# Optimization experiments

Hardware: AMD Instinct MI355X
Metric: run time of the kernel (lower is better)

## Reference

```python
import jax, jax.numpy as jnp
import numpy as np

B, T, D, K = 64, 4096, 128, 512

def setup_inputs() -> dict:
    key = jax.random.key(0)
    k1, k2, k3 = jax.random.split(key, 3)
    embeddings = jax.random.normal(k1, (B, T, D), dtype=jnp.float32)
    mask = jax.random.bernoulli(k2, 0.9, (B, T))
    W = jax.random.normal(k3, (D,), dtype=jnp.float32) * (1.0 / np.sqrt(D))
    b = jnp.zeros((1,), dtype=jnp.float32)
    return {"embeddings": embeddings, "mask": mask, "k": K, "W": W, "b": b}

def reference(embeddings, mask, k, W, b):
    batch, T, dim = embeddings.shape
    if k >= T:
        return embeddings, mask
    # linear score head: (B,T,D) @ (D,) + b -> (B,T)
    scores = jnp.einsum("btd,d->bt", embeddings, W) + b[0]
    neg_inf = jnp.array(-jnp.inf, dtype=scores.dtype)
    scores = jnp.where(mask, scores, neg_inf)
    soft_scores = jax.nn.sigmoid(scores)  # sigmoid(-inf) == 0
    _, topk_idx = jax.lax.top_k(scores, k)          # (B, k)
    topk_idx_sorted = jnp.sort(topk_idx, axis=1)    # preserve original token order
    rows = jnp.arange(batch)[:, None]
    hard_mask = jnp.zeros_like(scores).at[rows, topk_idx].set(1.0)
    # straight-through estimator: hard forward, soft gradient
    ste_mask = hard_mask - jax.lax.stop_gradient(soft_scores) + soft_scores
    weighted = embeddings * ste_mask[:, :, None]
    selected = jnp.take_along_axis(weighted, topk_idx_sorted[:, :, None], axis=1)  # (B,k,D)
    selected_mask = jnp.take_along_axis(mask, topk_idx_sorted, axis=1)             # (B,k)
    return selected, selected_mask
```

## Files before the change

kernel.cpp:

```cpp
#include <hip/hip_runtime.h>
#include <hip/hip_bf16.h>

#define BB 64
#define TT 4096
#define DD 128
#define KK 512

__global__ __launch_bounds__(256) void k_scores(
    const float* __restrict__ emb, const int* __restrict__ mask,
    const float* __restrict__ W, const float* __restrict__ bias,
    float* __restrict__ scores)
{
    const int wave = threadIdx.x >> 6;
    const int lane = threadIdx.x & 63;
    const int half = lane >> 5;
    const int sub  = lane & 31;
    const int pair0 = (blockIdx.x * 4 + wave) * 8;

    const float4 w = ((const float4*)W)[sub];
    const double w0 = (double)w.x, w1 = (double)w.y, w2 = (double)w.z, w3 = (double)w.w;
    const double b0 = (double)bias[0];

#pragma unroll
    for (int i = 0; i < 8; ++i) {
        const int t = (pair0 + i) * 2 + half;
        const float4 e = ((const float4*)emb)[(size_t)t * 32 + sub];
        double s = (double)e.x * w0 + (double)e.y * w1
                 + (double)e.z * w2 + (double)e.w * w3;
        s += __shfl_xor(s, 16, 64);
        s += __shfl_xor(s,  8, 64);
        s += __shfl_xor(s,  4, 64);
        s += __shfl_xor(s,  2, 64);
        s += __shfl_xor(s,  1, 64);
        if (sub == 0) {
            const float val = (float)(s + b0);
            scores[t] = mask[t] ? val : __uint_as_float(0xFF800000u);
        }
    }
}

__device__ __forceinline__ unsigned int block_incl_prefix(
    unsigned int v, int tid, volatile unsigned int* wsum)
{
    const int lane = tid & 63, wv = tid >> 6;
#pragma unroll
    for (int off = 1; off < 64; off <<= 1) {
        const unsigned int u = __shfl_up(v, off, 64);
        if (lane >= off) v += u;
    }
    if (lane == 63) wsum[wv] = v;
    __syncthreads();
    unsigned int add = 0;
    for (int w = 0; w < wv; ++w) add += wsum[w];
    v += add;
    __syncthreads();
    return v;
}

__global__ __launch_bounds__(256) void k_select(
    const float* __restrict__ scores, const int* __restrict__ mask,
    int* __restrict__ idx_out, float* __restrict__ mask_out)
{
    __shared__ unsigned int keys[TT];
    __shared__ unsigned int hist4[4][256];
    __shared__ unsigned int wsum[4];
    __shared__ unsigned int bcast[2];

    const int row = blockIdx.x;
    const int tid = threadIdx.x;
    const int wv  = tid >> 6;
    const float* srow = scores + (size_t)row * TT;
    const int*   mrow = mask   + (size_t)row * TT;

#pragma unroll
    for (int i = 0; i < 16; ++i) {
        const int t = tid * 16 + i;
        const unsigned int u = __float_as_uint(srow[t]);
        keys[t] = (u & 0x80000000u) ? ~u : (u | 0x80000000u);
    }

    unsigned int prefix = 0;
    unsigned int count_above = 0;
    for (int pass = 0; pass < 4; ++pass) {
        const int shift = 24 - 8 * pass;
#pragma unroll
        for (int w = 0; w < 4; ++w) hist4[w][tid] = 0;
        __syncthreads();
#pragma unroll
        for (int i = 0; i < 16; ++i) {
            const unsigned int k = keys[tid * 16 + i];
            const bool in_group = (pass == 0) || ((k >> (shift + 8)) == prefix);
            if (in_group) atomicAdd(&hist4[wv][(k >> shift) & 0xFFu], 1u);
        }
        __syncthreads();
        const unsigned int bin = 255u - (unsigned int)tid;
        const unsigned int h = hist4[0][bin] + hist4[1][bin]
                             + hist4[2][bin] + hist4[3][bin];
        const unsigned int incl = block_incl_prefix(h, tid, wsum);
        const unsigned int excl = incl - h;
        if (count_above + incl >= KK && count_above + excl < KK) {
            bcast[0] = bin;
            bcast[1] = count_above + excl;
        }
        __syncthreads();
        prefix = (prefix << 8) | bcast[0];
        count_above = bcast[1];
        __syncthreads();
    }
    const unsigned int vstar = prefix;
    const unsigned int need  = KK - count_above;

    unsigned int gt = 0, eq = 0;
#pragma unroll
    for (int i = 0; i < 16; ++i) {
        const unsigned int k = keys[tid * 16 + i];
        gt += (k > vstar);
        eq += (k == vstar);
    }
    const unsigned int packed = (gt << 16) | eq;
    const unsigned int incl2 = block_incl_prefix(packed, tid, wsum);
    const unsigned int before = incl2 - packed;
    unsigned int gt_b = before >> 16;
    unsigned int eq_b = before & 0xFFFFu;
#pragma unroll
    for (int i = 0; i < 16; ++i) {
        const int t = tid * 16 + i;
        const unsigned int k = keys[t];
        if (k > vstar) {
            const unsigned int pos = gt_b + (eq_b < need ? eq_b : need);
            idx_out[row * KK + pos]  = t;
            mask_out[row * KK + pos] = mrow[t] ? 1.0f : 0.0f;
            gt_b++;
        } else if (k == vstar) {
            if (eq_b < need) {
                const unsigned int pos = gt_b + eq_b;
                idx_out[row * KK + pos]  = t;
                mask_out[row * KK + pos] = mrow[t] ? 1.0f : 0.0f;
            }
            eq_b++;
        }
    }
}

__global__ __launch_bounds__(256) void k_gather(
    const float* __restrict__ emb, const int* __restrict__ idx,
    float* __restrict__ out)
{
    const int gp   = blockIdx.x * 8 + (threadIdx.x >> 5);
    const int lane = threadIdx.x & 31;
    const int b = gp >> 9;
    const int t = idx[gp];
    const float4* src = (const float4*)(emb + ((size_t)b * TT + t) * DD);
    float4*       dst = (float4*)(out + (size_t)gp * DD);
    dst[lane] = src[lane];
}

extern "C" void kernel_launch(void* const* d_in, const int* in_sizes, int n_in,
                              void* d_out, int out_size, void* d_ws, size_t ws_size,
                              hipStream_t stream)
{
    const float* emb  = (const float*)d_in[0];
    const int*   mask = (const int*)d_in[1];
    const float* W    = (const float*)d_in[3];
    const float* bias = (const float*)d_in[4];

    float* out_sel  = (float*)d_out;
    float* out_mask = (float*)d_out + (size_t)BB * KK * DD;

    float* scores = (float*)d_ws;
    int*   idx    = (int*)((char*)d_ws + (size_t)BB * TT * sizeof(float));

    k_scores<<<BB * TT / 64, 256, 0, stream>>>(emb, mask, W, bias, scores);
    k_select<<<BB, 256, 0, stream>>>(scores, mask, idx, out_mask);
    k_gather<<<BB * KK / 8, 256, 0, stream>>>(emb, idx, out_sel);
}
```

Baseline: 219.7 us.

## Widen radix-select block to 1024 threads and precompute sortable keys in score kernel

The score kernel now writes order-preserving unsigned keys directly, with masked tokens mapped to the key for -inf, so the select kernel no longer converts floats. The select kernel runs with 1024 threads per row, each handling 4 keys loaded as a single uint4. It uses 16 per-wave padded histograms reduced into one, and a single-wave scan over 256 bins. It also drops one barrier per pass. The aim is to cut the serial per-thread work in the 64-block select stage, which badly underfills the GPU, at the cost of more histogram reduction work and contention.

```diff
diff --git a/kernel.cpp b/kernel.cpp
--- a/kernel.cpp
+++ b/kernel.cpp
@@ -6,10 +6,12 @@
 #define DD 128
 #define KK 512
 
+#define KEY_NEG_INF 0x007FFFFFu
+
 __global__ __launch_bounds__(256) void k_scores(
     const float* __restrict__ emb, const int* __restrict__ mask,
     const float* __restrict__ W, const float* __restrict__ bias,
-    float* __restrict__ scores)
+    unsigned int* __restrict__ keys_out)
 {
     const int wave = threadIdx.x >> 6;
     const int lane = threadIdx.x & 63;
@@ -34,97 +36,111 @@
         s += __shfl_xor(s,  1, 64);
         if (sub == 0) {
             const float val = (float)(s + b0);
-            scores[t] = mask[t] ? val : __uint_as_float(0xFF800000u);
+            const unsigned int u = __float_as_uint(val);
+            unsigned int key = (u & 0x80000000u) ? ~u : (u | 0x80000000u);
+            if (!mask[t]) key = KEY_NEG_INF;
+            keys_out[t] = key;
         }
     }
 }
 
-__device__ __forceinline__ unsigned int block_incl_prefix(
-    unsigned int v, int tid, volatile unsigned int* wsum)
-{
-    const int lane = tid & 63, wv = tid >> 6;
-#pragma unroll
-    for (int off = 1; off < 64; off <<= 1) {
-        const unsigned int u = __shfl_up(v, off, 64);
-        if (lane >= off) v += u;
-    }
-    if (lane == 63) wsum[wv] = v;
-    __syncthreads();
-    unsigned int add = 0;
-    for (int w = 0; w < wv; ++w) add += wsum[w];
-    v += add;
-    __syncthreads();
-    return v;
-}
-
-__global__ __launch_bounds__(256) void k_select(
-    const float* __restrict__ scores, const int* __restrict__ mask,
+__global__ __launch_bounds__(1024) void k_select(
+    const unsigned int* __restrict__ keys_in, const int* __restrict__ mask,
     int* __restrict__ idx_out, float* __restrict__ mask_out)
 {
     __shared__ unsigned int keys[TT];
-    __shared__ unsigned int hist4[4][256];
-    __shared__ unsigned int wsum[4];
+    __shared__ unsigned int hist[16][257];
+    __shared__ unsigned int hist_final[256];
+    __shared__ unsigned int wsum[16];
     __shared__ unsigned int bcast[2];
 
-    const int row = blockIdx.x;
-    const int tid = threadIdx.x;
-    const int wv  = tid >> 6;
-    const float* srow = scores + (size_t)row * TT;
-    const int*   mrow = mask   + (size_t)row * TT;
+    const int row  = blockIdx.x;
+    const int tid  = threadIdx.x;
+    const int wv   = tid >> 6;
+    const int lane = tid & 63;
+    const unsigned int* krow = keys_in + (size_t)row * TT;
+    const int*          mrow = mask    + (size_t)row * TT;
 
-#pragma unroll
-    for (int i = 0; i < 16; ++i) {
-        const int t = tid * 16 + i;
-        const unsigned int u = __float_as_uint(srow[t]);
-        keys[t] = (u & 0x80000000u) ? ~u : (u | 0x80000000u);
-    }
+    const uint4 kv = ((const uint4*)krow)[tid];
+    ((uint4*)keys)[tid] = kv;
 
     unsigned int prefix = 0;
     unsigned int count_above = 0;
     for (int pass = 0; pass < 4; ++pass) {
         const int shift = 24 - 8 * pass;
-#pragma unroll
-        for (int w = 0; w < 4; ++w) hist4[w][tid] = 0;
+        for (int i = tid; i < 16 * 257; i += 1024) ((unsigned int*)hist)[i] = 0;
         __syncthreads();
 #pragma unroll
-        for (int i = 0; i < 16; ++i) {
-            const unsigned int k = keys[tid * 16 + i];
+        for (int i = 0; i < 4; ++i) {
+            const unsigned int k = keys[tid * 4 + i];
             const bool in_group = (pass == 0) || ((k >> (shift + 8)) == prefix);
-            if (in_group) atomicAdd(&hist4[wv][(k >> shift) & 0xFFu], 1u);
+            if (in_group) atomicAdd(&hist[wv][(k >> shift) & 0xFFu], 1u);
         }
         __syncthreads();
-        const unsigned int bin = 255u - (unsigned int)tid;
-        const unsigned int h = hist4[0][bin] + hist4[1][bin]
-                             + hist4[2][bin] + hist4[3][bin];
-        const unsigned int incl = block_incl_prefix(h, tid, wsum);
-        const unsigned int excl = incl - h;
-        if (count_above + incl >= KK && count_above + excl < KK) {
-            bcast[0] = bin;
-            bcast[1] = count_above + excl;
+        if (tid < 256) {
+            unsigned int s = 0;
+#pragma unroll
+            for (int w = 0; w < 16; ++w) s += hist[w][tid];
+            hist_final[tid] = s;
+        }
+        __syncthreads();
+        if (wv == 0) {
+            unsigned int v[4], c[4];
+            unsigned int run = 0;
+#pragma unroll
+            for (int j = 0; j < 4; ++j) {
+                v[j] = hist_final[255 - (4 * lane + j)];
+                run += v[j];
+                c[j] = run;
+            }
+            unsigned int scan = run;
+#pragma unroll
+            for (int off = 1; off < 64; off <<= 1) {
+                const unsigned int u = __shfl_up(scan, off, 64);
+                if (lane >= off) scan += u;
+            }
+            const unsigned int excl_w = scan - run;
+#pragma unroll
+            for (int j = 0; j < 4; ++j) {
+                const unsigned int incl = excl_w + c[j];
+                const unsigned int excl = incl - v[j];
+                if (count_above + incl >= KK && count_above + excl < KK) {
+                    bcast[0] = 255u - (unsigned int)(4 * lane + j);
+                    bcast[1] = count_above + excl;
+                }
+            }
         }
         __syncthreads();
         prefix = (prefix << 8) | bcast[0];
         count_above = bcast[1];
-        __syncthreads();
     }
     const unsigned int vstar = prefix;
     const unsigned int need  = KK - count_above;
 
     unsigned int gt = 0, eq = 0;
 #pragma unroll
-    for (int i = 0; i < 16; ++i) {
-        const unsigned int k = keys[tid * 16 + i];
+    for (int i = 0; i < 4; ++i) {
+        const unsigned int k = keys[tid * 4 + i];
         gt += (k > vstar);
         eq += (k == vstar);
     }
-    const unsigned int packed = (gt << 16) | eq;
-    const unsigned int incl2 = block_incl_prefix(packed, tid, wsum);
-    const unsigned int before = incl2 - packed;
+    unsigned int packed = (gt << 16) | eq;
+    unsigned int scan = packed;
+#pragma unroll
+    for (int off = 1; off < 64; off <<= 1) {
+        const unsigned int u = __shfl_up(scan, off, 64);
+        if (lane >= off) scan += u;
+    }
+    if (lane == 63) wsum[wv] = scan;
+    __syncthreads();
+    unsigned int add = 0;
+    for (int w = 0; w < wv; ++w) add += wsum[w];
+    const unsigned int before = scan - packed + add;
     unsigned int gt_b = before >> 16;
     unsigned int eq_b = before & 0xFFFFu;
 #pragma unroll
-    for (int i = 0; i < 16; ++i) {
-        const int t = tid * 16 + i;
+    for (int i = 0; i < 4; ++i) {
+        const int t = tid * 4 + i;
         const unsigned int k = keys[t];
         if (k > vstar) {
             const unsigned int pos = gt_b + (eq_b < need ? eq_b : need);
@@ -167,10 +183,10 @@
     float* out_sel  = (float*)d_out;
     float* out_mask = (float*)d_out + (size_t)BB * KK * DD;
 
-    float* scores = (float*)d_ws;
-    int*   idx    = (int*)((char*)d_ws + (size_t)BB * TT * sizeof(float));
+    unsigned int* keys = (unsigned int*)d_ws;
+    int*          idx  = (int*)((char*)d_ws + (size_t)BB * TT * sizeof(unsigned int));
 
-    k_scores<<<BB * TT / 64, 256, 0, stream>>>(emb, mask, W, bias, scores);
-    k_select<<<BB, 256, 0, stream>>>(scores, mask, idx, out_mask);
+    k_scores<<<BB * TT / 64, 256, 0, stream>>>(emb, mask, W, bias, keys);
+    k_select<<<BB, 1024, 0, stream>>>(keys, mask, idx, out_mask);
     k_gather<<<BB * KK / 8, 256, 0, stream>>>(emb, idx, out_sel);
 }
```

Result: faster. 212.9 us (-3.1%).
